# Kernel tuning notes

Hardware: AMD Instinct MI355X
Metric: run time of the kernel (lower is better)

## Reference

```python
import jax, jax.numpy as jnp
import numpy as np

N = 200000      # active voxels
CIN = 64
COUT = 128
L = 96
EPS = 1e-5

# 27 kernel offsets for a 3x3x3 sparse conv (Minkowski region: [-1,0,1]^3)
_OFFS = np.array([[dx, dy, dz] for dx in (-1, 0, 1) for dy in (-1, 0, 1) for dz in (-1, 0, 1)], dtype=np.int64)


def _build_nbr_map():
    """Build [27, N] map: nbr_idx[k, i] = row of input voxel at coord_i + off_k, or N if absent."""
    rng = np.random.default_rng(0)
    keys = rng.choice(L ** 3, size=N, replace=False)           # unique voxel hashes
    coords = np.stack(np.unravel_index(keys, (L, L, L)), axis=1).astype(np.int64)  # [N,3]
    order = np.argsort(keys)
    skeys = keys[order]
    maps = np.full((27, N), N, dtype=np.int32)
    for k in range(27):
        q = coords + _OFFS[k]
        inb = np.all((q >= 0) & (q < L), axis=1)
        qk = (q[:, 0] * L + q[:, 1]) * L + q[:, 2]
        pos = np.searchsorted(skeys, qk)
        pos = np.clip(pos, 0, N - 1)
        hit = inb & (skeys[pos] == qk)
        maps[k] = np.where(hit, order[pos].astype(np.int32), N)
    return jnp.asarray(maps)


def setup_inputs() -> dict:
    key = jax.random.key(0)
    ks = jax.random.split(key, 4)
    feats = jax.random.normal(ks[0], (N, CIN), dtype=jnp.float32)
    W1 = jax.random.normal(ks[1], (27, CIN, COUT), dtype=jnp.float32) * (1.0 / np.sqrt(27 * CIN))
    W2 = jax.random.normal(ks[2], (27, COUT, COUT), dtype=jnp.float32) * (1.0 / np.sqrt(27 * COUT))
    Wsk = jax.random.normal(ks[3], (CIN, COUT), dtype=jnp.float32) * (1.0 / np.sqrt(CIN))
    ones = jnp.ones((COUT,), jnp.float32)
    zeros = jnp.zeros((COUT,), jnp.float32)
    return {
        "feats": feats, "nbr_idx": _build_nbr_map(),
        "W1": W1, "g1": ones, "b1": zeros,
        "W2": W2, "g2": ones, "b2": zeros,
        "Wsk": Wsk, "gsk": ones, "bsk": zeros,
    }


def _sparse_conv3(feats, nbr_idx, W):
    """Stride-1 3x3x3 sparse conv: out[i] = sum_k feats[nbr(i,k)] @ W[k]."""
    fpad = jnp.concatenate([feats, jnp.zeros((1, feats.shape[1]), feats.dtype)], axis=0)  # sentinel row N -> 0
    out = jnp.zeros((feats.shape[0], W.shape[2]), feats.dtype)
    for k in range(W.shape[0]):  # fixed 27 kernel taps
        out = out + fpad[nbr_idx[k]] @ W[k]
    return out


def _bn(x, g, b):
    m = jnp.mean(x, axis=0)
    v = jnp.var(x, axis=0)
    return (x - m) * jax.lax.rsqrt(v + EPS) * g + b


def reference(feats, nbr_idx, W1, g1, b1, W2, g2, b2, Wsk, gsk, bsk):
    # skip branch: 1x1 sparse conv (pointwise matmul) + BN
    skip = _bn(feats @ Wsk, gsk, bsk)
    # res branch: conv3 -> BN -> conv3 -> BN
    h = _bn(_sparse_conv3(feats, nbr_idx, W1), g1, b1)
    res = _bn(_sparse_conv3(h, nbr_idx, W2), g2, b2)
    return jax.nn.relu(res + skip)
```

## Files before the change

### kernel.cpp

```cpp
#include <hip/hip_runtime.h>
#include <stdint.h>

#define NV 200000
#define BN_EPS 1e-5f

typedef short bf16x8 __attribute__((ext_vector_type(8)));
typedef float f32x4 __attribute__((ext_vector_type(4)));

__device__ inline unsigned short f2bf(float x) {
  union { float f; uint32_t u; } c; c.f = x;
  uint32_t r = c.u + 0x7fffu + ((c.u >> 16) & 1u);
  return (unsigned short)(r >> 16);
}
__device__ inline float bf2f(unsigned short u) {
  union { uint32_t u; float f; } c; c.u = ((uint32_t)u) << 16;
  return c.f;
}

__device__ inline void gload_lds16(const void* g, void* l) {
  __builtin_amdgcn_global_load_lds(
      (const __attribute__((address_space(1))) unsigned int*)(g),
      (__attribute__((address_space(3))) unsigned int*)(l), 16, 0, 0);
}

template <int K, int NTAPS, bool GATHER, bool OUTBF>
__global__ __launch_bounds__(256, 2) void conv_mfma(
    const unsigned short* __restrict__ Apad, const int* __restrict__ nbr,
    const unsigned short* __restrict__ Wpack, void* __restrict__ outp,
    float* __restrict__ ssum, float* __restrict__ ssq) {
  constexpr int S = K / 32;
  constexpr int TAPH = S * 8 * 64 * 8;
  constexpr int TAPBYTES = TAPH * 2;
  __shared__ unsigned short Wlds[2][TAPH];
  __shared__ float sred[4][128];

  const int tid = threadIdx.x;
  const int w = tid >> 6;
  const int l = tid & 63;
  const int l15 = l & 15;
  const int lhi = l >> 4;
  const int rowbase = blockIdx.x * 256 + w * 64;

  f32x4 acc[4][8];
#pragma unroll
  for (int rf = 0; rf < 4; ++rf)
#pragma unroll
    for (int cf = 0; cf < 8; ++cf) acc[rf][cf] = f32x4{0.f, 0.f, 0.f, 0.f};

  {
    const char* wsrc = (const char*)Wpack;
    const int base = w * (TAPBYTES / 4);
#pragma unroll
    for (int i = 0; i < TAPBYTES / 4096; ++i) {
      const int off = base + i * 1024;
      gload_lds16(wsrc + off + l * 16, (char*)(&Wlds[0][0]) + off);
    }
  }
  int ridx[4];
#pragma unroll
  for (int rf = 0; rf < 4; ++rf) {
    const int row = rowbase + rf * 16 + l15;
    int r = NV;
    if (row < NV) r = GATHER ? nbr[row] : row;
    ridx[rf] = r;
  }
  __syncthreads();

  for (int t = 0; t < NTAPS; ++t) {
    const int cur = t & 1;

    bf16x8 areg[4][S];
#pragma unroll
    for (int rf = 0; rf < 4; ++rf) {
      const unsigned short* ap = Apad + (size_t)ridx[rf] * K + lhi * 8;
#pragma unroll
      for (int s = 0; s < S; ++s)
        areg[rf][s] = *(const bf16x8*)(ap + s * 32);
    }

    if (t + 1 < NTAPS) {
      const char* wsrc = (const char*)Wpack + (size_t)(t + 1) * TAPBYTES;
      const int base = w * (TAPBYTES / 4);
#pragma unroll
      for (int i = 0; i < TAPBYTES / 4096; ++i) {
        const int off = base + i * 1024;
        gload_lds16(wsrc + off + l * 16, (char*)(&Wlds[cur ^ 1][0]) + off);
      }
    }

    int nr[4];
    if (GATHER && (t + 1 < NTAPS)) {
#pragma unroll
      for (int rf = 0; rf < 4; ++rf) {
        const int row = rowbase + rf * 16 + l15;
        int r = NV;
        if (row < NV) r = nbr[(size_t)(t + 1) * NV + row];
        nr[rf] = r;
      }
    }

    __builtin_amdgcn_s_setprio(1);
#pragma unroll
    for (int s = 0; s < S; ++s) {
      bf16x8 b[8];
#pragma unroll
      for (int cf = 0; cf < 8; ++cf)
        b[cf] = *(const bf16x8*)&Wlds[cur][((s * 8 + cf) * 64 + l) * 8];
#pragma unroll
      for (int rf = 0; rf < 4; ++rf)
#pragma unroll
        for (int cf = 0; cf < 8; ++cf)
          acc[rf][cf] = __builtin_amdgcn_mfma_f32_16x16x32_bf16(
              areg[rf][s], b[cf], acc[rf][cf], 0, 0, 0);
    }
    __builtin_amdgcn_s_setprio(0);

    __syncthreads();

    if (GATHER && (t + 1 < NTAPS)) {
#pragma unroll
      for (int rf = 0; rf < 4; ++rf) ridx[rf] = nr[rf];
    }
  }

  float psum[8], psq[8];
#pragma unroll
  for (int cf = 0; cf < 8; ++cf) {
    float s = 0.f, q = 0.f;
#pragma unroll
    for (int rf = 0; rf < 4; ++rf)
#pragma unroll
      for (int v = 0; v < 4; ++v) {
        const float x = acc[rf][cf][v];
        s += x;
        q += x * x;
      }
    psum[cf] = s;
    psq[cf] = q;
  }
#pragma unroll
  for (int cf = 0; cf < 8; ++cf) {
    psum[cf] += __shfl_xor(psum[cf], 16);
    psum[cf] += __shfl_xor(psum[cf], 32);
    psq[cf] += __shfl_xor(psq[cf], 16);
    psq[cf] += __shfl_xor(psq[cf], 32);
  }
  if (l < 16) {
#pragma unroll
    for (int cf = 0; cf < 8; ++cf) sred[w][cf * 16 + l] = psum[cf];
  }
  __syncthreads();
  if (tid < 128)
    atomicAdd(&ssum[tid], sred[0][tid] + sred[1][tid] + sred[2][tid] + sred[3][tid]);
  __syncthreads();
  if (l < 16) {
#pragma unroll
    for (int cf = 0; cf < 8; ++cf) sred[w][cf * 16 + l] = psq[cf];
  }
  __syncthreads();
  if (tid < 128)
    atomicAdd(&ssq[tid], sred[0][tid] + sred[1][tid] + sred[2][tid] + sred[3][tid]);

#pragma unroll
  for (int rf = 0; rf < 4; ++rf) {
#pragma unroll
    for (int v = 0; v < 4; ++v) {
      const int row = rowbase + rf * 16 + lhi * 4 + v;
      if (row < NV) {
#pragma unroll
        for (int cf = 0; cf < 8; ++cf) {
          const float x = acc[rf][cf][v];
          if (OUTBF)
            ((unsigned short*)outp)[(size_t)row * 128 + cf * 16 + l15] = f2bf(x);
          else
            ((float*)outp)[(size_t)row * 128 + cf * 16 + l15] = x;
        }
      }
    }
  }
}

__global__ void pack_w_kernel(const float* __restrict__ W,
                              unsigned short* __restrict__ o, int sshift,
                              int total) {
  const int e = blockIdx.x * blockDim.x + threadIdx.x;
  if (e >= total) return;
  const int j = e & 7;
  const int l = (e >> 3) & 63;
  const int cf = (e >> 9) & 7;
  const int ts = e >> 12;
  const int S = 1 << sshift;
  const int s = ts & (S - 1);
  const int tap = ts >> sshift;
  const int kk = s * 32 + (l >> 4) * 8 + j;
  const int col = cf * 16 + (l & 15);
  o[e] = f2bf(W[((size_t)tap * (S * 32) + kk) * 128 + col]);
}

__global__ void feats_to_bf16(const float* __restrict__ f,
                              unsigned short* __restrict__ o) {
  const int i = blockIdx.x * blockDim.x + threadIdx.x;
  if (i >= (NV + 1) * 16) return;
  const int row = i >> 4;
  const int c = (i & 15) * 4;
  ushort4 ov;
  if (row < NV) {
    const float4 v = *(const float4*)(f + (size_t)row * 64 + c);
    ov.x = f2bf(v.x);
    ov.y = f2bf(v.y);
    ov.z = f2bf(v.z);
    ov.w = f2bf(v.w);
  } else {
    ov = make_ushort4(0, 0, 0, 0);
  }
  *(ushort4*)(o + (size_t)row * 64 + c) = ov;
}

__global__ void zero_stats(float* st) {
  const int t = blockIdx.x * 256 + threadIdx.x;
  if (t < 768) st[t] = 0.f;
}

__global__ void finalize1(float* st, const float* g1, const float* b1,
                          const float* gsk, const float* bsk) {
  const float invN = 1.0f / NV;
  const int t = threadIdx.x;
  if (t < 128) {
    const float m = st[t] * invN;
    const float v = st[128 + t] * invN - m * m;
    const float sc = g1[t] * rsqrtf(v + BN_EPS);
    st[768 + t] = sc;
    st[896 + t] = b1[t] - m * sc;
  } else {
    const int c = t - 128;
    const float m = st[256 + c] * invN;
    const float v = st[384 + c] * invN - m * m;
    const float sc = gsk[c] * rsqrtf(v + BN_EPS);
    st[1024 + c] = sc;
    st[1152 + c] = bsk[c] - m * sc;
  }
}

__global__ void finalize2(float* st, const float* g2, const float* b2) {
  const float invN = 1.0f / NV;
  const int c = threadIdx.x;
  const float m = st[512 + c] * invN;
  const float v = st[640 + c] * invN - m * m;
  const float sc = g2[c] * rsqrtf(v + BN_EPS);
  st[1280 + c] = sc;
  st[1408 + c] = b2[c] - m * sc;
}

__global__ void bn_to_bf16(const unsigned short* __restrict__ raw,
                           const float* __restrict__ scale,
                           const float* __restrict__ bias,
                           unsigned short* __restrict__ outp) {
  const int i = blockIdx.x * blockDim.x + threadIdx.x;
  if (i >= (NV + 1) * 32) return;
  const int row = i >> 5;
  const int c = (i & 31) * 4;
  ushort4 ov;
  if (row < NV) {
    const ushort4 rv = *(const ushort4*)(raw + (size_t)row * 128 + c);
    ov.x = f2bf(bf2f(rv.x) * scale[c + 0] + bias[c + 0]);
    ov.y = f2bf(bf2f(rv.y) * scale[c + 1] + bias[c + 1]);
    ov.z = f2bf(bf2f(rv.z) * scale[c + 2] + bias[c + 2]);
    ov.w = f2bf(bf2f(rv.w) * scale[c + 3] + bias[c + 3]);
  } else {
    ov = make_ushort4(0, 0, 0, 0);
  }
  *(ushort4*)(outp + (size_t)row * 128 + c) = ov;
}

__global__ void final_kernel(float* __restrict__ outp,
                             const unsigned short* __restrict__ c2,
                             const unsigned short* __restrict__ sk,
                             const float* __restrict__ st) {
  const int i = blockIdx.x * blockDim.x + threadIdx.x;
  if (i >= NV * 32) return;
  const int row = i >> 5;
  const int c = (i & 31) * 4;
  const float* s2 = st + 1280;
  const float* b2 = st + 1408;
  const float* ss = st + 1024;
  const float* bs = st + 1152;
  const ushort4 rv = *(const ushort4*)(c2 + (size_t)row * 128 + c);
  const ushort4 kv = *(const ushort4*)(sk + (size_t)row * 128 + c);
  float4 o;
  o.x = fmaxf(0.f, bf2f(rv.x) * s2[c + 0] + b2[c + 0] + bf2f(kv.x) * ss[c + 0] + bs[c + 0]);
  o.y = fmaxf(0.f, bf2f(rv.y) * s2[c + 1] + b2[c + 1] + bf2f(kv.y) * ss[c + 1] + bs[c + 1]);
  o.z = fmaxf(0.f, bf2f(rv.z) * s2[c + 2] + b2[c + 2] + bf2f(kv.z) * ss[c + 2] + bs[c + 2]);
  o.w = fmaxf(0.f, bf2f(rv.w) * s2[c + 3] + b2[c + 3] + bf2f(kv.w) * ss[c + 3] + bs[c + 3]);
  *(float4*)(outp + (size_t)row * 128 + c) = o;
}

extern "C" void kernel_launch(void* const* d_in, const int* in_sizes, int n_in,
                              void* d_out, int out_size, void* d_ws,
                              size_t ws_size, hipStream_t stream) {
  const float* feats = (const float*)d_in[0];
  const int* nbr = (const int*)d_in[1];
  const float* W1 = (const float*)d_in[2];
  const float* g1 = (const float*)d_in[3];
  const float* b1 = (const float*)d_in[4];
  const float* W2 = (const float*)d_in[5];
  const float* g2 = (const float*)d_in[6];
  const float* b2 = (const float*)d_in[7];
  const float* Wsk = (const float*)d_in[8];
  const float* gsk = (const float*)d_in[9];
  const float* bsk = (const float*)d_in[10];

  char* ws = (char*)d_ws;
  auto align = [](size_t x) { return (x + 255) & ~(size_t)255; };
  size_t off = 0;
  float* stats = (float*)(ws + off);
  off = align(off + 12 * 128 * 4);
  unsigned short* w1p = (unsigned short*)(ws + off);
  off = align(off + (size_t)27 * 2 * 8 * 64 * 8 * 2);
  unsigned short* w2p = (unsigned short*)(ws + off);
  off = align(off + (size_t)27 * 4 * 8 * 64 * 8 * 2);
  unsigned short* wskp = (unsigned short*)(ws + off);
  off = align(off + (size_t)2 * 8 * 64 * 8 * 2);
  unsigned short* fbf = (unsigned short*)(ws + off);
  off = align(off + (size_t)(NV + 1) * 64 * 2);
  unsigned short* c1 = (unsigned short*)(ws + off);
  off = align(off + (size_t)NV * 128 * 2);
  unsigned short* skr = (unsigned short*)(ws + off);
  off = align(off + (size_t)NV * 128 * 2);
  unsigned short* hbf = (unsigned short*)(ws + off);
  off = align(off + (size_t)(NV + 1) * 128 * 2);

  float* out = (float*)d_out;

  zero_stats<<<3, 256, 0, stream>>>(stats);
  const int t1 = 27 * 2 * 8 * 64 * 8;
  pack_w_kernel<<<(t1 + 255) / 256, 256, 0, stream>>>(W1, w1p, 1, t1);
  const int t2 = 27 * 4 * 8 * 64 * 8;
  pack_w_kernel<<<(t2 + 255) / 256, 256, 0, stream>>>(W2, w2p, 2, t2);
  const int t3 = 2 * 8 * 64 * 8;
  pack_w_kernel<<<(t3 + 255) / 256, 256, 0, stream>>>(Wsk, wskp, 1, t3);
  feats_to_bf16<<<((NV + 1) * 16 + 255) / 256, 256, 0, stream>>>(feats, fbf);

  const int convBlocks = (NV + 255) / 256;
  conv_mfma<64, 27, true, true>
      <<<convBlocks, 256, 0, stream>>>(fbf, nbr, w1p, c1, stats + 0, stats + 128);
  conv_mfma<64, 1, false, true>
      <<<convBlocks, 256, 0, stream>>>(fbf, nullptr, wskp, skr, stats + 256, stats + 384);
  finalize1<<<1, 256, 0, stream>>>(stats, g1, b1, gsk, bsk);
  bn_to_bf16<<<((NV + 1) * 32 + 255) / 256, 256, 0, stream>>>(c1, stats + 768,
                                                              stats + 896, hbf);
  conv_mfma<128, 27, true, true>
      <<<convBlocks, 256, 0, stream>>>(hbf, nbr, w2p, c1, stats + 512, stats + 640);
  finalize2<<<1, 128, 0, stream>>>(stats, g2, b2);
  final_kernel<<<(NV * 32 + 255) / 256, 256, 0, stream>>>(out, c1, skr, stats);
}
```

Before: 522.0 us.

## Software-pipeline gathers with ping-pong A registers and split K into halves

Restructures the sparse-conv MFMA loop so the gather of the next step's A rows is issued before computing the current step, double-buffering A fragments in registers. The second conv splits K=128 into two 64-wide virtual taps, which halves the LDS weight stage per step and the register footprint per step. This overlaps global gather latency with MFMA work, at the cost of more registers held live, more loop steps and more barriers, and could hurt occupancy or cause spills.

```diff
diff --git a/kernel.cpp b/kernel.cpp
--- a/kernel.cpp
+++ b/kernel.cpp
@@ -23,13 +23,15 @@
       (__attribute__((address_space(3))) unsigned int*)(l), 16, 0, 0);
 }
 
-template <int K, int NTAPS, bool GATHER, bool OUTBF>
+template <int KV, int NTAPS, int KSPLIT, bool GATHER, bool OUTBF>
 __global__ __launch_bounds__(256, 2) void conv_mfma(
     const unsigned short* __restrict__ Apad, const int* __restrict__ nbr,
     const unsigned short* __restrict__ Wpack, void* __restrict__ outp,
     float* __restrict__ ssum, float* __restrict__ ssq) {
-  constexpr int S = K / 32;
-  constexpr int TAPH = S * 8 * 64 * 8;
+  constexpr int SV = KV / 32;
+  constexpr int K = KV * KSPLIT;
+  constexpr int NVT = NTAPS * KSPLIT;
+  constexpr int TAPH = SV * 8 * 64 * 8;
   constexpr int TAPBYTES = TAPH * 2;
   __shared__ unsigned short Wlds[2][TAPH];
   __shared__ float sred[4][128];
@@ -47,81 +49,99 @@
 #pragma unroll
     for (int cf = 0; cf < 8; ++cf) acc[rf][cf] = f32x4{0.f, 0.f, 0.f, 0.f};
 
-  {
-    const char* wsrc = (const char*)Wpack;
+  bf16x8 aregA[4][SV], aregB[4][SV];
+  int idxc[4];
+  int idxn[4];
+
+  auto stageW = [&](int v, int buf) {
+    const char* wsrc = (const char*)Wpack + (size_t)v * TAPBYTES;
     const int base = w * (TAPBYTES / 4);
 #pragma unroll
     for (int i = 0; i < TAPBYTES / 4096; ++i) {
       const int off = base + i * 1024;
-      gload_lds16(wsrc + off + l * 16, (char*)(&Wlds[0][0]) + off);
-    }
-  }
-  int ridx[4];
-#pragma unroll
-  for (int rf = 0; rf < 4; ++rf) {
-    const int row = rowbase + rf * 16 + l15;
-    int r = NV;
-    if (row < NV) r = GATHER ? nbr[row] : row;
-    ridx[rf] = r;
-  }
-  __syncthreads();
-
-  for (int t = 0; t < NTAPS; ++t) {
-    const int cur = t & 1;
-
-    bf16x8 areg[4][S];
+      gload_lds16(wsrc + off + l * 16, (char*)(&Wlds[buf][0]) + off);
+    }
+  };
+  auto loadIdx = [&](int rt, int (&d)[4]) {
 #pragma unroll
     for (int rf = 0; rf < 4; ++rf) {
-      const unsigned short* ap = Apad + (size_t)ridx[rf] * K + lhi * 8;
-#pragma unroll
-      for (int s = 0; s < S; ++s)
-        areg[rf][s] = *(const bf16x8*)(ap + s * 32);
-    }
-
-    if (t + 1 < NTAPS) {
-      const char* wsrc = (const char*)Wpack + (size_t)(t + 1) * TAPBYTES;
-      const int base = w * (TAPBYTES / 4);
-#pragma unroll
-      for (int i = 0; i < TAPBYTES / 4096; ++i) {
-        const int off = base + i * 1024;
-        gload_lds16(wsrc + off + l * 16, (char*)(&Wlds[cur ^ 1][0]) + off);
-      }
-    }
-
-    int nr[4];
-    if (GATHER && (t + 1 < NTAPS)) {
-#pragma unroll
-      for (int rf = 0; rf < 4; ++rf) {
-        const int row = rowbase + rf * 16 + l15;
-        int r = NV;
-        if (row < NV) r = nbr[(size_t)(t + 1) * NV + row];
-        nr[rf] = r;
-      }
-    }
-
+      const int row = rowbase + rf * 16 + l15;
+      int r = NV;
+      if (row < NV) r = GATHER ? nbr[(size_t)rt * NV + row] : row;
+      d[rf] = r;
+    }
+  };
+  auto gathers = [&](bf16x8 (&ar)[4][SV], const int (&ri)[4], int voff) {
+#pragma unroll
+    for (int rf = 0; rf < 4; ++rf) {
+      const unsigned short* ap = Apad + (size_t)ri[rf] * K + voff + lhi * 8;
+#pragma unroll
+      for (int s = 0; s < SV; ++s) ar[rf][s] = *(const bf16x8*)(ap + s * 32);
+    }
+  };
+  auto compute = [&](bf16x8 (&ar)[4][SV], int buf) {
     __builtin_amdgcn_s_setprio(1);
 #pragma unroll
-    for (int s = 0; s < S; ++s) {
+    for (int s = 0; s < SV; ++s) {
       bf16x8 b[8];
 #pragma unroll
       for (int cf = 0; cf < 8; ++cf)
-        b[cf] = *(const bf16x8*)&Wlds[cur][((s * 8 + cf) * 64 + l) * 8];
+        b[cf] = *(const bf16x8*)&Wlds[buf][((s * 8 + cf) * 64 + l) * 8];
 #pragma unroll
       for (int rf = 0; rf < 4; ++rf)
 #pragma unroll
         for (int cf = 0; cf < 8; ++cf)
           acc[rf][cf] = __builtin_amdgcn_mfma_f32_16x16x32_bf16(
-              areg[rf][s], b[cf], acc[rf][cf], 0, 0, 0);
+              ar[rf][s], b[cf], acc[rf][cf], 0, 0, 0);
     }
     __builtin_amdgcn_s_setprio(0);
-
+  };
+
+  auto body = [&](int v, bf16x8 (&arC)[4][SV], bf16x8 (&arN)[4][SV],
+                  bool nxtOdd) {
+    const int vn = v + 1;
+    if (vn < NVT) {
+      stageW(vn, vn & 1);
+      if constexpr (KSPLIT == 2) {
+        if (nxtOdd) {
+          gathers(arN, idxc, KV);
+          if constexpr (GATHER) {
+            const int rt1 = (vn >> 1) + 1;
+            if (rt1 < NTAPS) loadIdx(rt1, idxn);
+          }
+        } else {
+#pragma unroll
+          for (int rf = 0; rf < 4; ++rf) idxc[rf] = idxn[rf];
+          gathers(arN, idxc, 0);
+        }
+      } else {
+        if constexpr (GATHER) {
+#pragma unroll
+          for (int rf = 0; rf < 4; ++rf) idxc[rf] = idxn[rf];
+        }
+        gathers(arN, idxc, 0);
+        if constexpr (GATHER) {
+          if (vn + 1 < NVT) loadIdx(vn + 1, idxn);
+        }
+      }
+    }
+    compute(arC, v & 1);
     __syncthreads();
-
-    if (GATHER && (t + 1 < NTAPS)) {
-#pragma unroll
-      for (int rf = 0; rf < 4; ++rf) ridx[rf] = nr[rf];
-    }
-  }
+  };
+
+  loadIdx(0, idxc);
+  stageW(0, 0);
+  gathers(aregA, idxc, 0);
+  if constexpr (GATHER && KSPLIT == 1) {
+    if (NVT > 1) loadIdx(1, idxn);
+  }
+  __syncthreads();
+
+  for (int v = 0; v + 1 < NVT; v += 2) {
+    body(v, aregA, aregB, true);
+    body(v + 1, aregB, aregA, false);
+  }
+  if constexpr (NVT & 1) body(NVT - 1, aregA, aregB, true);
 
   float psum[8], psq[8];
 #pragma unroll
@@ -341,14 +361,14 @@
   feats_to_bf16<<<((NV + 1) * 16 + 255) / 256, 256, 0, stream>>>(feats, fbf);
 
   const int convBlocks = (NV + 255) / 256;
-  conv_mfma<64, 27, true, true>
+  conv_mfma<64, 27, 1, true, true>
       <<<convBlocks, 256, 0, stream>>>(fbf, nbr, w1p, c1, stats + 0, stats + 128);
-  conv_mfma<64, 1, false, true>
+  conv_mfma<64, 1, 1, false, true>
       <<<convBlocks, 256, 0, stream>>>(fbf, nullptr, wskp, skr, stats + 256, stats + 384);
   finalize1<<<1, 256, 0, stream>>>(stats, g1, b1, gsk, bsk);
   bn_to_bf16<<<((NV + 1) * 32 + 255) / 256, 256, 0, stream>>>(c1, stats + 768,
                                                               stats + 896, hbf);
-  conv_mfma<128, 27, true, true>
+  conv_mfma<64, 27, 2, true, true>
       <<<convBlocks, 256, 0, stream>>>(hbf, nbr, w2p, c1, stats + 512, stats + 640);
   finalize2<<<1, 128, 0, stream>>>(stats, g2, b2);
   final_kernel<<<(NV * 32 + 255) / 256, 256, 0, stream>>>(out, c1, skr, stats);
```

Result: slower. 975.0 us (+86.8%).

## Software-pipeline gathers one stage ahead with double-buffered A registers and K-split stages

Applied to the files above, without the earlier changes.

Restructures the sparse-conv MFMA loop so the gather of the next stage's activation rows is issued before computing the current stage. Two register sets (aregA/aregB) alternate, which hides gather latency behind MFMA work. For the 128-channel conv, each tap is split into two 64-channel halves so the LDS weight stage stays at 32 KB and the same pipeline applies. The cost is higher register pressure from the extra A buffers, which could cut occupancy or cause spills, and twice as many barriers for the second conv.

```diff
diff --git a/kernel.cpp b/kernel.cpp
--- a/kernel.cpp
+++ b/kernel.cpp
@@ -23,13 +23,59 @@
       (__attribute__((address_space(3))) unsigned int*)(l), 16, 0, 0);
 }
 
-template <int K, int NTAPS, bool GATHER, bool OUTBF>
+
+#define STAGEW(v, buf)                                                       \
+  do {                                                                       \
+    const char* wsrc_ = (const char*)Wpack + (size_t)(v)*TAPBYTES;           \
+    _Pragma("unroll") for (int i_ = 0; i_ < TAPBYTES / 4096; ++i_) {         \
+      const int off_ = w * (TAPBYTES / 4) + i_ * 1024;                       \
+      gload_lds16(wsrc_ + off_ + l * 16, (char*)(&Wlds[buf][0]) + off_);     \
+    }                                                                        \
+  } while (0)
+
+#define LOADIDX(rt, d)                                                       \
+  do {                                                                       \
+    _Pragma("unroll") for (int rf_ = 0; rf_ < 4; ++rf_) {                    \
+      const int row_ = rowbase + rf_ * 16 + l15;                             \
+      int r_ = NV;                                                           \
+      if (row_ < NV) r_ = GATHER ? nbr[(size_t)(rt)*NV + row_] : row_;       \
+      d[rf_] = r_;                                                           \
+    }                                                                        \
+  } while (0)
+
+#define GATHERS(ar, idx, voff)                                               \
+  do {                                                                       \
+    _Pragma("unroll") for (int rf_ = 0; rf_ < 4; ++rf_) {                    \
+      const unsigned short* ap_ =                                            \
+          Apad + (size_t)idx[rf_] * K + (voff) + lhi * 8;                    \
+      _Pragma("unroll") for (int s_ = 0; s_ < 2; ++s_) ar[rf_][s_] =         \
+          *(const bf16x8*)(ap_ + s_ * 32);                                   \
+    }                                                                        \
+  } while (0)
+
+#define COMPUTE(ar, buf)                                                     \
+  do {                                                                       \
+    __builtin_amdgcn_s_setprio(1);                                           \
+    _Pragma("unroll") for (int s_ = 0; s_ < 2; ++s_) {                       \
+      bf16x8 b_[8];                                                          \
+      _Pragma("unroll") for (int cf_ = 0; cf_ < 8; ++cf_) b_[cf_] =          \
+          *(const bf16x8*)&Wlds[buf][((s_ * 8 + cf_) * 64 + l) * 8];         \
+      _Pragma("unroll") for (int rf_ = 0; rf_ < 4; ++rf_)                    \
+          _Pragma("unroll") for (int cf_ = 0; cf_ < 8; ++cf_) acc[rf_][cf_] =\
+          __builtin_amdgcn_mfma_f32_16x16x32_bf16(ar[rf_][s_], b_[cf_],      \
+                                                  acc[rf_][cf_], 0, 0, 0);   \
+    }                                                                        \
+    __builtin_amdgcn_s_setprio(0);                                           \
+  } while (0)
+
+template <int NTAPS, int KSPLIT, bool GATHER, bool OUTBF>
 __global__ __launch_bounds__(256, 2) void conv_mfma(
     const unsigned short* __restrict__ Apad, const int* __restrict__ nbr,
     const unsigned short* __restrict__ Wpack, void* __restrict__ outp,
     float* __restrict__ ssum, float* __restrict__ ssq) {
-  constexpr int S = K / 32;
-  constexpr int TAPH = S * 8 * 64 * 8;
+  constexpr int KV = 64;
+  constexpr int K = KV * KSPLIT;
+  constexpr int TAPH = 2 * 8 * 64 * 8;
   constexpr int TAPBYTES = TAPH * 2;
   __shared__ unsigned short Wlds[2][TAPH];
   __shared__ float sred[4][128];
@@ -47,79 +93,52 @@
 #pragma unroll
     for (int cf = 0; cf < 8; ++cf) acc[rf][cf] = f32x4{0.f, 0.f, 0.f, 0.f};
 
-  {
-    const char* wsrc = (const char*)Wpack;
-    const int base = w * (TAPBYTES / 4);
-#pragma unroll
-    for (int i = 0; i < TAPBYTES / 4096; ++i) {
-      const int off = base + i * 1024;
-      gload_lds16(wsrc + off + l * 16, (char*)(&Wlds[0][0]) + off);
+  bf16x8 aregA[4][2], aregB[4][2];
+  int idxA[4], idxB[4];
+
+  if constexpr (KSPLIT == 1) {
+    LOADIDX(0, idxA);
+    STAGEW(0, 0);
+    GATHERS(aregA, idxA, 0);
+    if (NTAPS > 1) LOADIDX(1, idxB);
+    __syncthreads();
+    for (int t = 0; t < NTAPS; t += 2) {
+      if (t + 1 < NTAPS) {
+        STAGEW(t + 1, 1);
+        GATHERS(aregB, idxB, 0);
+        if (t + 2 < NTAPS) LOADIDX(t + 2, idxA);
+      }
+      COMPUTE(aregA, 0);
+      __syncthreads();
+      if (t + 1 < NTAPS) {
+        if (t + 2 < NTAPS) {
+          STAGEW(t + 2, 0);
+          GATHERS(aregA, idxA, 0);
+          if (t + 3 < NTAPS) LOADIDX(t + 3, idxB);
+        }
+        COMPUTE(aregB, 1);
+        __syncthreads();
+      }
     }
-  }
-  int ridx[4];
-#pragma unroll
-  for (int rf = 0; rf < 4; ++rf) {
-    const int row = rowbase + rf * 16 + l15;
-    int r = NV;
-    if (row < NV) r = GATHER ? nbr[row] : row;
-    ridx[rf] = r;
-  }
-  __syncthreads();
-
-  for (int t = 0; t < NTAPS; ++t) {
-    const int cur = t & 1;
-
-    bf16x8 areg[4][S];
-#pragma unroll
-    for (int rf = 0; rf < 4; ++rf) {
-      const unsigned short* ap = Apad + (size_t)ridx[rf] * K + lhi * 8;
-#pragma unroll
-      for (int s = 0; s < S; ++s)
-        areg[rf][s] = *(const bf16x8*)(ap + s * 32);
-    }
-
-    if (t + 1 < NTAPS) {
-      const char* wsrc = (const char*)Wpack + (size_t)(t + 1) * TAPBYTES;
-      const int base = w * (TAPBYTES / 4);
-#pragma unroll
-      for (int i = 0; i < TAPBYTES / 4096; ++i) {
-        const int off = base + i * 1024;
-        gload_lds16(wsrc + off + l * 16, (char*)(&Wlds[cur ^ 1][0]) + off);
-      }
-    }
-
-    int nr[4];
-    if (GATHER && (t + 1 < NTAPS)) {
-#pragma unroll
-      for (int rf = 0; rf < 4; ++rf) {
-        const int row = rowbase + rf * 16 + l15;
-        int r = NV;
-        if (row < NV) r = nbr[(size_t)(t + 1) * NV + row];
-        nr[rf] = r;
-      }
-    }
-
-    __builtin_amdgcn_s_setprio(1);
-#pragma unroll
-    for (int s = 0; s < S; ++s) {
-      bf16x8 b[8];
-#pragma unroll
-      for (int cf = 0; cf < 8; ++cf)
-        b[cf] = *(const bf16x8*)&Wlds[cur][((s * 8 + cf) * 64 + l) * 8];
-#pragma unroll
-      for (int rf = 0; rf < 4; ++rf)
-#pragma unroll
-        for (int cf = 0; cf < 8; ++cf)
-          acc[rf][cf] = __builtin_amdgcn_mfma_f32_16x16x32_bf16(
-              areg[rf][s], b[cf], acc[rf][cf], 0, 0, 0);
-    }
-    __builtin_amdgcn_s_setprio(0);
-
+  } else {
+    LOADIDX(0, idxA);
+    STAGEW(0, 0);
+    GATHERS(aregA, idxA, 0);
     __syncthreads();
-
-    if (GATHER && (t + 1 < NTAPS)) {
-#pragma unroll
-      for (int rf = 0; rf < 4; ++rf) ridx[rf] = nr[rf];
+    for (int rt = 0; rt < NTAPS; ++rt) {
+      STAGEW(2 * rt + 1, 1);
+      GATHERS(aregB, idxA, KV);
+      if (rt + 1 < NTAPS) LOADIDX(rt + 1, idxB);
+      COMPUTE(aregA, 0);
+      __syncthreads();
+      if (rt + 1 < NTAPS) {
+        STAGEW(2 * rt + 2, 0);
+        GATHERS(aregA, idxB, 0);
+#pragma unroll
+        for (int rf = 0; rf < 4; ++rf) idxA[rf] = idxB[rf];
+      }
+      COMPUTE(aregB, 1);
+      __syncthreads();
     }
   }
 
@@ -341,14 +360,14 @@
   feats_to_bf16<<<((NV + 1) * 16 + 255) / 256, 256, 0, stream>>>(feats, fbf);
 
   const int convBlocks = (NV + 255) / 256;
-  conv_mfma<64, 27, true, true>
+  conv_mfma<27, 1, true, true>
       <<<convBlocks, 256, 0, stream>>>(fbf, nbr, w1p, c1, stats + 0, stats + 128);
-  conv_mfma<64, 1, false, true>
+  conv_mfma<1, 1, false, true>
       <<<convBlocks, 256, 0, stream>>>(fbf, nullptr, wskp, skr, stats + 256, stats + 384);
   finalize1<<<1, 256, 0, stream>>>(stats, g1, b1, gsk, bsk);
   bn_to_bf16<<<((NV + 1) * 32 + 255) / 256, 256, 0, stream>>>(c1, stats + 768,
                                                               stats + 896, hbf);
-  conv_mfma<128, 27, true, true>
+  conv_mfma<27, 2, true, true>
       <<<convBlocks, 256, 0, stream>>>(hbf, nbr, w2p, c1, stats + 512, stats + 640);
   finalize2<<<1, 128, 0, stream>>>(stats, g2, b2);
   final_kernel<<<(NV * 32 + 255) / 256, 256, 0, stream>>>(out, c1, skr, stats);
```

Result: no change. 522.4 us (+0.1%).
